# Performance work log

Measured on AMD Instinct MI355X. Metric: run time of the kernel, lower is better.

Reference implementation:

```python
import jax, jax.numpy as jnp
import numpy as np

EMBED_DIM = 1024
NUM_HEADS = 16
HEAD_DIM = EMBED_DIM // NUM_HEADS
WINDOW = 256
B, S = 2, 2048


def setup_inputs() -> dict:
    key = jax.random.key(0)
    ks = jax.random.split(key, 9)
    sc = 1.0 / np.sqrt(EMBED_DIM)
    inp = {
        "x": jax.random.normal(ks[0], (B, S, EMBED_DIM), dtype=jnp.float32),
        "Wq": jax.random.normal(ks[1], (EMBED_DIM, EMBED_DIM), dtype=jnp.float32) * sc,
        "Wk": jax.random.normal(ks[2], (EMBED_DIM, EMBED_DIM), dtype=jnp.float32) * sc,
        "Wv": jax.random.normal(ks[3], (EMBED_DIM, EMBED_DIM), dtype=jnp.float32) * sc,
        "Wo": jax.random.normal(ks[4], (EMBED_DIM, EMBED_DIM), dtype=jnp.float32) * sc,
        "bq": jax.random.normal(ks[5], (EMBED_DIM,), dtype=jnp.float32) * 0.01,
        "bk": jax.random.normal(ks[6], (EMBED_DIM,), dtype=jnp.float32) * 0.01,
        "bv": jax.random.normal(ks[7], (EMBED_DIM,), dtype=jnp.float32) * 0.01,
        "bo": jax.random.normal(ks[8], (EMBED_DIM,), dtype=jnp.float32) * 0.01,
    }
    return inp


def _sliding_window_mask(seq_len: int) -> jnp.ndarray:
    # True where attention is NOT permitted (future or beyond window)
    idx = jnp.arange(seq_len)
    rel = idx[None, :] - idx[:, None]  # (S, S): key_pos - query_pos
    return (rel > 0) | (rel < -WINDOW)


def reference(x, Wq, Wk, Wv, Wo, bq, bk, bv, bo):
    Bx, Sx, E = x.shape
    H, D = NUM_HEADS, HEAD_DIM
    # projections (torch Linear: y = x @ W.T + b)
    q = (x @ Wq.T + bq).reshape(Bx, Sx, H, D).transpose(0, 2, 1, 3)  # (B,H,S,D)
    k = (x @ Wk.T + bk).reshape(Bx, Sx, H, D).transpose(0, 2, 1, 3)
    v = (x @ Wv.T + bv).reshape(Bx, Sx, H, D).transpose(0, 2, 1, 3)
    q = q * (D ** -0.5)
    attn = jnp.einsum("bhqd,bhkd->bhqk", q, k)  # (B,H,S,S) dense scores
    mask = _sliding_window_mask(Sx)
    attn = jnp.where(mask, -jnp.inf, attn)
    attn = jax.nn.softmax(attn, axis=-1)
    y = jnp.einsum("bhqk,bhkd->bhqd", attn, v)
    y = y.transpose(0, 2, 1, 3).reshape(Bx, Sx, E)
    return y @ Wo.T + bo
```

## Files before the change

kernel.cpp:

```cpp
#include <hip/hip_runtime.h>

#define E_DIM 1024
#define NHEAD 16
#define HDIM 64
#define SEQ 2048
#define NBATCH 2
#define WIN 256
#define MTOK (NBATCH * SEQ)

typedef __attribute__((ext_vector_type(4))) float f32x4;
typedef __attribute__((ext_vector_type(8))) short short8;
typedef __attribute__((ext_vector_type(4))) unsigned short u16x4;

#define AS1 __attribute__((address_space(1)))
#define AS3 __attribute__((address_space(3)))

__device__ __forceinline__ void gll16(const void* g, void* l) {
    __builtin_amdgcn_global_load_lds((const AS1 void*)g, (AS3 void*)l, 16, 0, 0);
}

__device__ __forceinline__ unsigned short f2bf(float f) {
    union { float f; unsigned u; } a; a.f = f;
    unsigned r = a.u + 0x7fffu + ((a.u >> 16) & 1u);
    return (unsigned short)(r >> 16);
}

__global__ __launch_bounds__(256) void conv_f2b(const float* __restrict__ src,
                                                unsigned short* __restrict__ dst, int n4) {
    int i = blockIdx.x * 256 + threadIdx.x;
    int stride = gridDim.x * 256;
    for (; i < n4; i += stride) {
        float4 v = ((const float4*)src)[i];
        u16x4 o;
        o[0] = f2bf(v.x); o[1] = f2bf(v.y); o[2] = f2bf(v.z); o[3] = f2bf(v.w);
        ((u16x4*)dst)[i] = o;
    }
}

__device__ __forceinline__ void gemm_tile(const unsigned short* __restrict__ A,
                                          const unsigned short* __restrict__ Bw,
                                          int m0, int n0,
                                          f32x4 acc[4][4], char* ldsA, char* ldsB) {
    const int t = threadIdx.x;
    const int w = t >> 6, l = t & 63;
    const int r16 = l & 15, kq = l >> 4;
    const int wr = w >> 1, wc = w & 1;
    const int srow = l >> 3, ps = l & 7;

    for (int kt = 0; kt < E_DIM / 64; ++kt) {
        #pragma unroll
        for (int c = 0; c < 4; ++c) {
            int chunk = w * 4 + c;
            int row = chunk * 8 + srow;
            int kslot = ps ^ (row & 7);
            gll16(A  + (size_t)(m0 + row) * E_DIM + kt * 64 + kslot * 8, ldsA + chunk * 1024);
            gll16(Bw + (size_t)(n0 + row) * E_DIM + kt * 64 + kslot * 8, ldsB + chunk * 1024);
        }
        __syncthreads();
        #pragma unroll
        for (int kk = 0; kk < 2; ++kk) {
            short8 af[4], bfr[4];
            #pragma unroll
            for (int m = 0; m < 4; ++m) {
                int rr = wr * 64 + m * 16 + r16;
                int c = kk * 4 + kq;
                af[m] = *(const short8*)(ldsA + rr * 128 + ((c ^ (rr & 7)) * 16));
            }
            #pragma unroll
            for (int n = 0; n < 4; ++n) {
                int rr = wc * 64 + n * 16 + r16;
                int c = kk * 4 + kq;
                bfr[n] = *(const short8*)(ldsB + rr * 128 + ((c ^ (rr & 7)) * 16));
            }
            #pragma unroll
            for (int m = 0; m < 4; ++m)
                #pragma unroll
                for (int n = 0; n < 4; ++n)
                    acc[m][n] = __builtin_amdgcn_mfma_f32_16x16x32_bf16(af[m], bfr[n], acc[m][n], 0, 0, 0);
        }
        __syncthreads();
    }
}

__global__ __launch_bounds__(256) void gemm_qkv(const unsigned short* __restrict__ xb,
        const unsigned short* __restrict__ wqb, const unsigned short* __restrict__ wkb,
        const unsigned short* __restrict__ wvb,
        const float* __restrict__ bq, const float* __restrict__ bk, const float* __restrict__ bv,
        unsigned short* __restrict__ qo, unsigned short* __restrict__ ko, unsigned short* __restrict__ vo) {
    __shared__ char lds[32768];
    const int m0 = blockIdx.x * 128;
    const int by = blockIdx.y;
    const int mat = by >> 3;
    const int nb0 = (by & 7) * 128;
    const unsigned short* Bw = (mat == 0) ? wqb : (mat == 1) ? wkb : wvb;
    const float* bias = (mat == 0) ? bq : (mat == 1) ? bk : bv;
    unsigned short* dst = (mat == 0) ? qo : (mat == 1) ? ko : vo;
    const float scale = (mat == 0) ? 0.125f : 1.0f;

    f32x4 acc[4][4];
    #pragma unroll
    for (int m = 0; m < 4; ++m)
        #pragma unroll
        for (int n = 0; n < 4; ++n)
            acc[m][n] = (f32x4){0.f, 0.f, 0.f, 0.f};

    gemm_tile(xb, Bw, m0, nb0, acc, lds, lds + 16384);

    const int t = threadIdx.x;
    const int w = t >> 6, l = t & 63;
    const int r16 = l & 15, kq = l >> 4;
    const int wr = w >> 1, wc = w & 1;
    #pragma unroll
    for (int n = 0; n < 4; ++n) {
        int e = nb0 + wc * 64 + n * 16 + r16;
        float bb = bias[e];
        int h = e >> 6, d = e & 63;
        #pragma unroll
        for (int m = 0; m < 4; ++m) {
            #pragma unroll
            for (int r = 0; r < 4; ++r) {
                int tok = m0 + wr * 64 + m * 16 + kq * 4 + r;
                int b = tok >> 11, s = tok & (SEQ - 1);
                float val = (acc[m][n][r] + bb) * scale;
                dst[((size_t)(b * NHEAD + h) * SEQ + s) * HDIM + d] = f2bf(val);
            }
        }
    }
}

__global__ __launch_bounds__(256) void transpose_v(const unsigned short* __restrict__ v,
                                                   unsigned short* __restrict__ vT) {
    __shared__ unsigned short tile[64][72];
    const int bh = blockIdx.x >> 5;
    const int s0 = (blockIdx.x & 31) * 64;
    const int t = threadIdx.x;
    const int rr = t >> 3;
    const int c8 = (t & 7) * 8;
    #pragma unroll
    for (int i = 0; i < 2; ++i) {
        int s = i * 32 + rr;
        short8 vv = *(const short8*)(v + ((size_t)bh * SEQ + s0 + s) * HDIM + c8);
        #pragma unroll
        for (int j = 0; j < 8; ++j) tile[s][c8 + j] = (unsigned short)vv[j];
    }
    __syncthreads();
    #pragma unroll
    for (int i = 0; i < 2; ++i) {
        int d = i * 32 + rr;
        short8 ov;
        #pragma unroll
        for (int j = 0; j < 8; ++j) ov[j] = (short)tile[c8 + j][d];
        *(short8*)(vT + ((size_t)bh * HDIM + d) * SEQ + s0 + c8) = ov;
    }
}

__global__ __launch_bounds__(256) void attn_swa(const unsigned short* __restrict__ q,
                                                const unsigned short* __restrict__ k,
                                                const unsigned short* __restrict__ vT,
                                                unsigned short* __restrict__ y) {
    __shared__ char plds[4 * 2048];
    const int t = threadIdx.x;
    const int w = t >> 6, l = t & 63;
    const int r16 = l & 15, kq = l >> 4;
    const int wid = blockIdx.x * 4 + w;
    const int bh = wid >> 7;
    const int q0 = (wid & 127) * 16;
    const unsigned short* qp = q + (size_t)bh * SEQ * HDIM;
    const unsigned short* kp = k + (size_t)bh * SEQ * HDIM;
    const unsigned short* vp = vT + (size_t)bh * HDIM * SEQ;
    char* pl = plds + w * 2048;

    short8 qf0 = *(const short8*)(qp + (q0 + r16) * HDIM + kq * 8);
    short8 qf1 = *(const short8*)(qp + (q0 + r16) * HDIM + 32 + kq * 8);

    f32x4 po[4];
    #pragma unroll
    for (int nn = 0; nn < 4; ++nn) po[nn] = (f32x4){0.f, 0.f, 0.f, 0.f};
    float mrow[4] = {-1e30f, -1e30f, -1e30f, -1e30f};
    float lrow[4] = {0.f, 0.f, 0.f, 0.f};

    const int kstart = (q0 >= WIN) ? ((q0 - WIN) & ~31) : 0;
    for (int k0 = kstart; k0 <= q0 + 15; k0 += 32) {
        f32x4 sc[2];
        #pragma unroll
        for (int n = 0; n < 2; ++n) {
            const unsigned short* kr = kp + (size_t)(k0 + n * 16 + r16) * HDIM + kq * 8;
            short8 kf0 = *(const short8*)(kr);
            short8 kf1 = *(const short8*)(kr + 32);
            f32x4 z = {0.f, 0.f, 0.f, 0.f};
            z = __builtin_amdgcn_mfma_f32_16x16x32_bf16(qf0, kf0, z, 0, 0, 0);
            sc[n] = __builtin_amdgcn_mfma_f32_16x16x32_bf16(qf1, kf1, z, 0, 0, 0);
        }
        float tmax[4];
        #pragma unroll
        for (int r = 0; r < 4; ++r) {
            int qrow = q0 + kq * 4 + r;
            int key0 = k0 + r16;
            int key1 = key0 + 16;
            if (!(key0 <= qrow && key0 >= qrow - WIN)) sc[0][r] = -1e30f;
            if (!(key1 <= qrow && key1 >= qrow - WIN)) sc[1][r] = -1e30f;
            tmax[r] = fmaxf(sc[0][r], sc[1][r]);
        }
        #pragma unroll
        for (int off = 1; off < 16; off <<= 1) {
            #pragma unroll
            for (int r = 0; r < 4; ++r)
                tmax[r] = fmaxf(tmax[r], __shfl_xor(tmax[r], off));
        }
        float pv0[4], pv1[4], psum[4];
        #pragma unroll
        for (int r = 0; r < 4; ++r) {
            float mnew = fmaxf(mrow[r], tmax[r]);
            float resc = __expf(mrow[r] - mnew);
            mrow[r] = mnew;
            lrow[r] *= resc;
            po[0][r] *= resc; po[1][r] *= resc; po[2][r] *= resc; po[3][r] *= resc;
            float p0 = (sc[0][r] > -1e29f) ? __expf(sc[0][r] - mnew) : 0.f;
            float p1 = (sc[1][r] > -1e29f) ? __expf(sc[1][r] - mnew) : 0.f;
            pv0[r] = p0; pv1[r] = p1;
            psum[r] = p0 + p1;
        }
        #pragma unroll
        for (int off = 1; off < 16; off <<= 1) {
            #pragma unroll
            for (int r = 0; r < 4; ++r)
                psum[r] += __shfl_xor(psum[r], off);
        }
        #pragma unroll
        for (int r = 0; r < 4; ++r) lrow[r] += psum[r];

        #pragma unroll
        for (int r = 0; r < 4; ++r) {
            int row = kq * 4 + r;
            int c0 = r16 ^ ((row & 7) << 3);
            int c1 = (16 + r16) ^ ((row & 7) << 3);
            *(unsigned short*)(pl + row * 128 + c0 * 2) = f2bf(pv0[r]);
            *(unsigned short*)(pl + row * 128 + c1 * 2) = f2bf(pv1[r]);
        }
        short8 pa = *(const short8*)(pl + r16 * 128 + ((kq ^ (r16 & 7)) * 16));
        #pragma unroll
        for (int nn = 0; nn < 4; ++nn) {
            short8 vf = *(const short8*)(vp + (size_t)(nn * 16 + r16) * SEQ + k0 + kq * 8);
            po[nn] = __builtin_amdgcn_mfma_f32_16x16x32_bf16(pa, vf, po[nn], 0, 0, 0);
        }
    }

    const int b = bh >> 4, h = bh & 15;
    #pragma unroll
    for (int nn = 0; nn < 4; ++nn) {
        #pragma unroll
        for (int r = 0; r < 4; ++r) {
            int s = q0 + kq * 4 + r;
            float val = po[nn][r] / lrow[r];
            y[((size_t)(b * SEQ + s)) * E_DIM + h * HDIM + nn * 16 + r16] = f2bf(val);
        }
    }
}

__global__ __launch_bounds__(256) void gemm_out(const unsigned short* __restrict__ yb,
        const unsigned short* __restrict__ wob, const float* __restrict__ bo,
        float* __restrict__ out) {
    __shared__ char lds[32768];
    const int m0 = blockIdx.x * 128;
    const int n0 = blockIdx.y * 128;
    f32x4 acc[4][4];
    #pragma unroll
    for (int m = 0; m < 4; ++m)
        #pragma unroll
        for (int n = 0; n < 4; ++n)
            acc[m][n] = (f32x4){0.f, 0.f, 0.f, 0.f};

    gemm_tile(yb, wob, m0, n0, acc, lds, lds + 16384);

    const int t = threadIdx.x;
    const int w = t >> 6, l = t & 63;
    const int r16 = l & 15, kq = l >> 4;
    const int wr = w >> 1, wc = w & 1;
    #pragma unroll
    for (int n = 0; n < 4; ++n) {
        int e = n0 + wc * 64 + n * 16 + r16;
        float bb = bo[e];
        #pragma unroll
        for (int m = 0; m < 4; ++m) {
            #pragma unroll
            for (int r = 0; r < 4; ++r) {
                int tok = m0 + wr * 64 + m * 16 + kq * 4 + r;
                out[(size_t)tok * E_DIM + e] = acc[m][n][r] + bb;
            }
        }
    }
}

extern "C" void kernel_launch(void* const* d_in, const int* in_sizes, int n_in,
                              void* d_out, int out_size, void* d_ws, size_t ws_size,
                              hipStream_t stream) {
    const float* x  = (const float*)d_in[0];
    const float* Wq = (const float*)d_in[1];
    const float* Wk = (const float*)d_in[2];
    const float* Wv = (const float*)d_in[3];
    const float* Wo = (const float*)d_in[4];
    const float* bq = (const float*)d_in[5];
    const float* bk = (const float*)d_in[6];
    const float* bv = (const float*)d_in[7];
    const float* bo = (const float*)d_in[8];
    float* out = (float*)d_out;

    char* ws = (char*)d_ws;
    unsigned short* xb  = (unsigned short*)(ws);
    unsigned short* wqb = (unsigned short*)(ws + ((size_t)8 << 20));
    unsigned short* wkb = (unsigned short*)(ws + ((size_t)10 << 20));
    unsigned short* wvb = (unsigned short*)(ws + ((size_t)12 << 20));
    unsigned short* wob = (unsigned short*)(ws + ((size_t)14 << 20));
    unsigned short* qw  = (unsigned short*)(ws + ((size_t)16 << 20));
    unsigned short* kw  = (unsigned short*)(ws + ((size_t)24 << 20));
    unsigned short* vw  = (unsigned short*)(ws + ((size_t)32 << 20));
    unsigned short* vTw = (unsigned short*)(ws + ((size_t)40 << 20));
    unsigned short* yw  = (unsigned short*)(ws + ((size_t)48 << 20));

    conv_f2b<<<4096, 256, 0, stream>>>(x, xb, MTOK * E_DIM / 4);
    conv_f2b<<<1024, 256, 0, stream>>>(Wq, wqb, E_DIM * E_DIM / 4);
    conv_f2b<<<1024, 256, 0, stream>>>(Wk, wkb, E_DIM * E_DIM / 4);
    conv_f2b<<<1024, 256, 0, stream>>>(Wv, wvb, E_DIM * E_DIM / 4);
    conv_f2b<<<1024, 256, 0, stream>>>(Wo, wob, E_DIM * E_DIM / 4);

    gemm_qkv<<<dim3(32, 24), 256, 0, stream>>>(xb, wqb, wkb, wvb, bq, bk, bv, qw, kw, vw);
    transpose_v<<<1024, 256, 0, stream>>>(vw, vTw);
    attn_swa<<<1024, 256, 0, stream>>>(qw, kw, vTw, yw);
    gemm_out<<<dim3(32, 8), 256, 0, stream>>>(yw, wob, bo, out);
}
```

Baseline: 201.8 us.

## Replace QKV GEMM with pipelined 256x256 tile kernel writing transposed V directly

Replaces the QKV projection GEMM with a 512-thread, 256x256-tile kernel that uses a 4-stage LDS ring buffer loaded via global_load_lds, with interleaved barriers and priority hints so loads overlap MFMA work. The V output is written directly in transposed layout, which removes the separate transpose kernel and its extra global round trip. The four weight conversions are merged into one launch. The larger tiles mean only 192 blocks for the GEMM, which may underfill the GPU, and the unswizzled 64-byte LDS rows may cause bank conflicts.

```diff
diff --git a/kernel.cpp b/kernel.cpp
--- a/kernel.cpp
+++ b/kernel.cpp
@@ -7,6 +7,8 @@
 #define NBATCH 2
 #define WIN 256
 #define MTOK (NBATCH * SEQ)
+#define BKT 32
+#define NT (E_DIM / BKT)
 
 typedef __attribute__((ext_vector_type(4))) float f32x4;
 typedef __attribute__((ext_vector_type(8))) short short8;
@@ -37,6 +39,130 @@
     }
 }
 
+__global__ __launch_bounds__(256) void conv_w4(const float* __restrict__ w0, const float* __restrict__ w1,
+                                               const float* __restrict__ w2, const float* __restrict__ w3,
+                                               unsigned short* __restrict__ o0, unsigned short* __restrict__ o1,
+                                               unsigned short* __restrict__ o2, unsigned short* __restrict__ o3) {
+    const int m = blockIdx.y;
+    const float* src = (m == 0) ? w0 : (m == 1) ? w1 : (m == 2) ? w2 : w3;
+    unsigned short* dst = (m == 0) ? o0 : (m == 1) ? o1 : (m == 2) ? o2 : o3;
+    int i = blockIdx.x * 256 + threadIdx.x;
+    float4 v = ((const float4*)src)[i];
+    u16x4 o;
+    o[0] = f2bf(v.x); o[1] = f2bf(v.y); o[2] = f2bf(v.z); o[3] = f2bf(v.w);
+    ((u16x4*)dst)[i] = o;
+}
+
+__global__ __launch_bounds__(512, 2) void gemm8_qkv(const unsigned short* __restrict__ xb,
+        const unsigned short* __restrict__ wqb, const unsigned short* __restrict__ wkb,
+        const unsigned short* __restrict__ wvb,
+        const float* __restrict__ bq, const float* __restrict__ bk, const float* __restrict__ bv,
+        unsigned short* __restrict__ qo, unsigned short* __restrict__ ko,
+        unsigned short* __restrict__ vTo) {
+    __shared__ char lds[131072];
+    const int tid = threadIdx.x;
+    const int w = tid >> 6, l = tid & 63;
+    const int r16 = l & 15, kq = l >> 4;
+    const int wm = w >> 2, wn = w & 3;
+    const int m0 = blockIdx.x * 256;
+    const int by = blockIdx.y;
+    const int mat = by >> 2;
+    const int nb = (by & 3) * 256;
+    const unsigned short* Bw = (mat == 0) ? wqb : (mat == 1) ? wkb : wvb;
+
+    const int srow = tid >> 2;
+    const int sslot = tid & 3;
+    const unsigned short* aSrc0 = xb + (size_t)(m0 + srow) * E_DIM + sslot * 8;
+    const unsigned short* aSrc1 = aSrc0 + (size_t)128 * E_DIM;
+    const unsigned short* bSrc0 = Bw + (size_t)(nb + srow) * E_DIM + sslot * 8;
+    const unsigned short* bSrc1 = bSrc0 + (size_t)128 * E_DIM;
+    const int dstOff = w * 1024;
+
+#define STAGE_A(t) { char* d_ = lds + ((t) & 3) * 32768 + dstOff; \
+                     gll16(aSrc0 + (t) * BKT, d_); gll16(aSrc1 + (t) * BKT, d_ + 8192); }
+#define STAGE_B(t) { char* d_ = lds + ((t) & 3) * 32768 + 16384 + dstOff; \
+                     gll16(bSrc0 + (t) * BKT, d_); gll16(bSrc1 + (t) * BKT, d_ + 8192); }
+
+    f32x4 acc[8][4];
+    #pragma unroll
+    for (int m = 0; m < 8; ++m)
+        #pragma unroll
+        for (int n = 0; n < 4; ++n)
+            acc[m][n] = (f32x4){0.f, 0.f, 0.f, 0.f};
+
+    STAGE_A(0); STAGE_B(0); STAGE_A(1); STAGE_B(1);
+
+    for (int t = 0; t < NT; ++t) {
+        if (t < NT - 1) { asm volatile("s_waitcnt vmcnt(4)" ::: "memory"); }
+        else            { asm volatile("s_waitcnt vmcnt(0)" ::: "memory"); }
+        __builtin_amdgcn_sched_barrier(0);
+        __builtin_amdgcn_s_barrier();
+        __builtin_amdgcn_sched_barrier(0);
+        char* la = lds + (t & 3) * 32768;
+        char* lb = la + 16384;
+        short8 bfr[4], af[4];
+        #pragma unroll
+        for (int n = 0; n < 4; ++n)
+            bfr[n] = *(const short8*)(lb + (wn * 64 + n * 16 + r16) * 64 + kq * 16);
+        #pragma unroll
+        for (int j = 0; j < 4; ++j)
+            af[j] = *(const short8*)(la + (wm * 128 + j * 16 + r16) * 64 + kq * 16);
+        if (t + 2 < NT) STAGE_A(t + 2);
+        __builtin_amdgcn_s_barrier();
+        __builtin_amdgcn_sched_barrier(0);
+        __builtin_amdgcn_s_setprio(1);
+        #pragma unroll
+        for (int j = 0; j < 4; ++j)
+            #pragma unroll
+            for (int n = 0; n < 4; ++n)
+                acc[j][n] = __builtin_amdgcn_mfma_f32_16x16x32_bf16(af[j], bfr[n], acc[j][n], 0, 0, 0);
+        __builtin_amdgcn_s_setprio(0);
+        short8 af2[4];
+        #pragma unroll
+        for (int j = 0; j < 4; ++j)
+            af2[j] = *(const short8*)(la + (wm * 128 + (4 + j) * 16 + r16) * 64 + kq * 16);
+        if (t + 2 < NT) STAGE_B(t + 2);
+        __builtin_amdgcn_s_barrier();
+        __builtin_amdgcn_sched_barrier(0);
+        __builtin_amdgcn_s_setprio(1);
+        #pragma unroll
+        for (int j = 0; j < 4; ++j)
+            #pragma unroll
+            for (int n = 0; n < 4; ++n)
+                acc[4 + j][n] = __builtin_amdgcn_mfma_f32_16x16x32_bf16(af2[j], bfr[n], acc[4 + j][n], 0, 0, 0);
+        __builtin_amdgcn_s_setprio(0);
+    }
+#undef STAGE_A
+#undef STAGE_B
+
+    const float* bias = (mat == 0) ? bq : (mat == 1) ? bk : bv;
+    const float scale = (mat == 0) ? 0.125f : 1.0f;
+    #pragma unroll
+    for (int n = 0; n < 4; ++n) {
+        int e = nb + wn * 64 + n * 16 + r16;
+        float bb = bias[e];
+        int h = e >> 6, d = e & 63;
+        #pragma unroll
+        for (int m = 0; m < 8; ++m) {
+            int tok = m0 + wm * 128 + m * 16 + kq * 4;
+            int b = tok >> 11, s = tok & (SEQ - 1);
+            if (mat == 2) {
+                u16x4 o;
+                #pragma unroll
+                for (int r = 0; r < 4; ++r) o[r] = f2bf(acc[m][n][r] + bb);
+                *(u16x4*)(vTo + ((size_t)(b * NHEAD + h) * HDIM + d) * SEQ + s) = o;
+            } else {
+                unsigned short* dst = (mat == 0) ? qo : ko;
+                #pragma unroll
+                for (int r = 0; r < 4; ++r) {
+                    float val = (acc[m][n][r] + bb) * scale;
+                    dst[((size_t)(b * NHEAD + h) * SEQ + s + r) * HDIM + d] = f2bf(val);
+                }
+            }
+        }
+    }
+}
+
 __device__ __forceinline__ void gemm_tile(const unsigned short* __restrict__ A,
                                           const unsigned short* __restrict__ Bw,
                                           int m0, int n0,
@@ -79,78 +205,6 @@
                     acc[m][n] = __builtin_amdgcn_mfma_f32_16x16x32_bf16(af[m], bfr[n], acc[m][n], 0, 0, 0);
         }
         __syncthreads();
-    }
-}
-
-__global__ __launch_bounds__(256) void gemm_qkv(const unsigned short* __restrict__ xb,
-        const unsigned short* __restrict__ wqb, const unsigned short* __restrict__ wkb,
-        const unsigned short* __restrict__ wvb,
-        const float* __restrict__ bq, const float* __restrict__ bk, const float* __restrict__ bv,
-        unsigned short* __restrict__ qo, unsigned short* __restrict__ ko, unsigned short* __restrict__ vo) {
-    __shared__ char lds[32768];
-    const int m0 = blockIdx.x * 128;
-    const int by = blockIdx.y;
-    const int mat = by >> 3;
-    const int nb0 = (by & 7) * 128;
-    const unsigned short* Bw = (mat == 0) ? wqb : (mat == 1) ? wkb : wvb;
-    const float* bias = (mat == 0) ? bq : (mat == 1) ? bk : bv;
-    unsigned short* dst = (mat == 0) ? qo : (mat == 1) ? ko : vo;
-    const float scale = (mat == 0) ? 0.125f : 1.0f;
-
-    f32x4 acc[4][4];
-    #pragma unroll
-    for (int m = 0; m < 4; ++m)
-        #pragma unroll
-        for (int n = 0; n < 4; ++n)
-            acc[m][n] = (f32x4){0.f, 0.f, 0.f, 0.f};
-
-    gemm_tile(xb, Bw, m0, nb0, acc, lds, lds + 16384);
-
-    const int t = threadIdx.x;
-    const int w = t >> 6, l = t & 63;
-    const int r16 = l & 15, kq = l >> 4;
-    const int wr = w >> 1, wc = w & 1;
-    #pragma unroll
-    for (int n = 0; n < 4; ++n) {
-        int e = nb0 + wc * 64 + n * 16 + r16;
-        float bb = bias[e];
-        int h = e >> 6, d = e & 63;
-        #pragma unroll
-        for (int m = 0; m < 4; ++m) {
-            #pragma unroll
-            for (int r = 0; r < 4; ++r) {
-                int tok = m0 + wr * 64 + m * 16 + kq * 4 + r;
-                int b = tok >> 11, s = tok & (SEQ - 1);
-                float val = (acc[m][n][r] + bb) * scale;
-                dst[((size_t)(b * NHEAD + h) * SEQ + s) * HDIM + d] = f2bf(val);
-            }
-        }
-    }
-}
-
-__global__ __launch_bounds__(256) void transpose_v(const unsigned short* __restrict__ v,
-                                                   unsigned short* __restrict__ vT) {
-    __shared__ unsigned short tile[64][72];
-    const int bh = blockIdx.x >> 5;
-    const int s0 = (blockIdx.x & 31) * 64;
-    const int t = threadIdx.x;
-    const int rr = t >> 3;
-    const int c8 = (t & 7) * 8;
-    #pragma unroll
-    for (int i = 0; i < 2; ++i) {
-        int s = i * 32 + rr;
-        short8 vv = *(const short8*)(v + ((size_t)bh * SEQ + s0 + s) * HDIM + c8);
-        #pragma unroll
-        for (int j = 0; j < 8; ++j) tile[s][c8 + j] = (unsigned short)vv[j];
-    }
-    __syncthreads();
-    #pragma unroll
-    for (int i = 0; i < 2; ++i) {
-        int d = i * 32 + rr;
-        short8 ov;
-        #pragma unroll
-        for (int j = 0; j < 8; ++j) ov[j] = (short)tile[c8 + j][d];
-        *(short8*)(vT + ((size_t)bh * HDIM + d) * SEQ + s0 + c8) = ov;
     }
 }
 
@@ -313,18 +367,13 @@
     unsigned short* wob = (unsigned short*)(ws + ((size_t)14 << 20));
     unsigned short* qw  = (unsigned short*)(ws + ((size_t)16 << 20));
     unsigned short* kw  = (unsigned short*)(ws + ((size_t)24 << 20));
-    unsigned short* vw  = (unsigned short*)(ws + ((size_t)32 << 20));
     unsigned short* vTw = (unsigned short*)(ws + ((size_t)40 << 20));
     unsigned short* yw  = (unsigned short*)(ws + ((size_t)48 << 20));
 
     conv_f2b<<<4096, 256, 0, stream>>>(x, xb, MTOK * E_DIM / 4);
-    conv_f2b<<<1024, 256, 0, stream>>>(Wq, wqb, E_DIM * E_DIM / 4);
-    conv_f2b<<<1024, 256, 0, stream>>>(Wk, wkb, E_DIM * E_DIM / 4);
-    conv_f2b<<<1024, 256, 0, stream>>>(Wv, wvb, E_DIM * E_DIM / 4);
-    conv_f2b<<<1024, 256, 0, stream>>>(Wo, wob, E_DIM * E_DIM / 4);
-
-    gemm_qkv<<<dim3(32, 24), 256, 0, stream>>>(xb, wqb, wkb, wvb, bq, bk, bv, qw, kw, vw);
-    transpose_v<<<1024, 256, 0, stream>>>(vw, vTw);
+    conv_w4<<<dim3(1024, 4), 256, 0, stream>>>(Wq, Wk, Wv, Wo, wqb, wkb, wvb, wob);
+
+    gemm8_qkv<<<dim3(16, 12), 512, 0, stream>>>(xb, wqb, wkb, wvb, bq, bk, bv, qw, kw, vTw);
     attn_swa<<<1024, 256, 0, stream>>>(qw, kw, vTw, yw);
     gemm_out<<<dim3(32, 8), 256, 0, stream>>>(yw, wob, bo, out);
 }
```

Measured after the change: 188.0 us. 1.07x faster.
